# Performance work log

Measured on AMD Instinct MI355X. Metric: run time of the kernel, lower is better.

Reference implementation:

```python
import jax, jax.numpy as jnp
import numpy as np

N = 50000      # nodes
E = 800000     # edges (before self-loops)
F_IN = 128     # num_node_features
H = 4          # heads
C = 64         # hidden_channels
G = 64         # graphs in batch
OUT = 5


def setup_inputs():
    key = jax.random.key(0)
    ks = jax.random.split(key, 16)
    s = 0.1
    def rn(k, shape, sc=s):
        return jax.random.normal(k, shape, dtype=jnp.float32) * sc
    return {
        "x": rn(ks[0], (N, F_IN), 1.0),
        "edge_index": jax.random.randint(ks[1], (2, E), 0, N, dtype=jnp.int32),
        "batch": jnp.sort(jax.random.randint(ks[2], (N,), 0, G, dtype=jnp.int32)),
        "W1": rn(ks[3], (F_IN, H * C)), "a1s": rn(ks[4], (H, C)), "a1d": rn(ks[5], (H, C)), "b1": jnp.zeros((H * C,), jnp.float32),
        "g1": jnp.ones((H * C,), jnp.float32), "be1": jnp.zeros((H * C,), jnp.float32),
        "W2": rn(ks[6], (H * C, H * C)), "a2s": rn(ks[7], (H, C)), "a2d": rn(ks[8], (H, C)), "b2": jnp.zeros((H * C,), jnp.float32),
        "g2": jnp.ones((H * C,), jnp.float32), "be2": jnp.zeros((H * C,), jnp.float32),
        "W3": rn(ks[9], (H * C, C)), "a3s": rn(ks[10], (1, C)), "a3d": rn(ks[11], (1, C)), "b3": jnp.zeros((C,), jnp.float32),
        "g3": jnp.ones((C,), jnp.float32), "be3": jnp.zeros((C,), jnp.float32),
        "Wg": rn(ks[12], (C, 128)), "bg": jnp.zeros((128,), jnp.float32),
        "Wg2": rn(ks[13], (128, 64)), "bg2": jnp.zeros((64,), jnp.float32),
        "Wo": rn(ks[14], (64, OUT)), "bo": jnp.zeros((OUT,), jnp.float32),
    }


def _layer_norm(x, g, b, eps=1e-5):
    mu = jnp.mean(x, axis=-1, keepdims=True)
    var = jnp.mean((x - mu) ** 2, axis=-1, keepdims=True)
    return (x - mu) * jax.lax.rsqrt(var + eps) * g + b


def _gat_conv(x, src, dst, W, a_s, a_d, b, heads, c, concat):
    # PyG GATConv (eval mode, dropout inactive): linear -> per-edge scores ->
    # segment softmax over incoming edges of each dst -> scatter-sum aggregation.
    n = x.shape[0]
    h = (x @ W).reshape(n, heads, c)                 # [N,H,C]
    alpha_src = jnp.sum(h * a_s, axis=-1)            # [N,H]
    alpha_dst = jnp.sum(h * a_d, axis=-1)            # [N,H]
    e = jax.nn.leaky_relu(alpha_src[src] + alpha_dst[dst], 0.2)   # [E',H]
    emax = jax.ops.segment_max(e, dst, num_segments=n)            # [N,H]
    ex = jnp.exp(e - emax[dst])
    denom = jax.ops.segment_sum(ex, dst, num_segments=n)
    alpha = ex / denom[dst]                          # softmax per dst (self-loops guarantee denom>0)
    out = jax.ops.segment_sum(alpha[:, :, None] * h[src], dst, num_segments=n)  # [N,H,C]
    out = out.reshape(n, heads * c) if concat else out.mean(axis=1)
    return out + b


def reference(x, edge_index, batch, W1, a1s, a1d, b1, g1, be1, W2, a2s, a2d, b2, g2, be2, W3, a3s, a3d, b3, g3, be3, Wg, bg, Wg2, bg2, Wo, bo):
    n = x.shape[0]
    loop = jnp.arange(n, dtype=edge_index.dtype)
    src = jnp.concatenate([edge_index[0], loop])     # GATConv adds self-loops
    dst = jnp.concatenate([edge_index[1], loop])
    h = _gat_conv(x, src, dst, W1, a1s, a1d, b1, H, C, True)
    h = jax.nn.elu(_layer_norm(h, g1, be1))
    h = _gat_conv(h, src, dst, W2, a2s, a2d, b2, H, C, True)
    h = jax.nn.elu(_layer_norm(h, g2, be2))
    h = _gat_conv(h, src, dst, W3, a3s, a3d, b3, 1, C, False)
    h = jax.nn.elu(_layer_norm(h, g3, be3))
    # global_mean_pool over graph ids
    sums = jax.ops.segment_sum(h, batch, num_segments=G)
    cnt = jax.ops.segment_sum(jnp.ones((n,), h.dtype), batch, num_segments=G)
    gm = sums / jnp.maximum(cnt, 1.0)[:, None]
    z = jax.nn.relu(gm @ Wg + bg)
    z = jax.nn.relu(z @ Wg2 + bg2)
    return z @ Wo + bo
```

## Files before the change

### kernel.cpp

```cpp
#include <hip/hip_runtime.h>
#include <math.h>

typedef _Float16 half2v __attribute__((ext_vector_type(2)));
typedef _Float16 half4v __attribute__((ext_vector_type(4)));
typedef _Float16 half8v __attribute__((ext_vector_type(8)));
typedef float floatx4 __attribute__((ext_vector_type(4)));

static __device__ __forceinline__ half2v pack_rtz(float a, float b) {
  return __builtin_bit_cast(half2v, __builtin_amdgcn_cvt_pkrtz(a, b));
}

__global__ void cvt16_kernel(const float* __restrict__ in, _Float16* __restrict__ out, int n8) {
  int i = blockIdx.x * 256 + threadIdx.x;
  if (i >= n8) return;
  float4 a = ((const float4*)in)[2 * i];
  float4 b = ((const float4*)in)[2 * i + 1];
  half8v h = {(_Float16)a.x, (_Float16)a.y, (_Float16)a.z, (_Float16)a.w,
              (_Float16)b.x, (_Float16)b.y, (_Float16)b.z, (_Float16)b.w};
  ((half8v*)out)[i] = h;
}

__global__ void wt_kernel(const float* __restrict__ W, _Float16* __restrict__ Wt, int K, int Nc) {
  int col = blockIdx.x;
  int k = threadIdx.x;
  if (k < K) Wt[(size_t)col * K + k] = (_Float16)W[(size_t)k * Nc + col];
}

__global__ void count_kernel(const int* __restrict__ ei, int E, int N, int* __restrict__ counts) {
  int e = blockIdx.x * 256 + threadIdx.x;
  if (e >= E + N) return;
  int d = (e < E) ? ei[E + e] : (e - E);
  atomicAdd(&counts[d], 1);
}

__global__ __launch_bounds__(1024) void scan1_kernel(const int* __restrict__ counts,
                                                     int* __restrict__ offsets,
                                                     int* __restrict__ blocksums, int n) {
  __shared__ int wsum[16];
  int tid = threadIdx.x, lane = tid & 63, wid = tid >> 6;
  int i = blockIdx.x * 1024 + tid;
  int v = (i < n) ? counts[i] : 0;
  int x = v;
  #pragma unroll
  for (int off = 1; off < 64; off <<= 1) {
    int t = __shfl_up(x, off);
    if (lane >= off) x += t;
  }
  if (lane == 63) wsum[wid] = x;
  __syncthreads();
  if (wid == 0) {
    int w = (lane < 16) ? wsum[lane] : 0;
    #pragma unroll
    for (int off = 1; off < 16; off <<= 1) {
      int t = __shfl_up(w, off);
      if (lane >= off) w += t;
    }
    if (lane < 16) wsum[lane] = w;
  }
  __syncthreads();
  int wpre = (wid > 0) ? wsum[wid - 1] : 0;
  if (i < n) offsets[i] = wpre + x - v;
  if (tid == 0) blocksums[blockIdx.x] = wsum[15];
}

__global__ __launch_bounds__(1024) void scan2_kernel(int* __restrict__ blocksums,
                                                     int* __restrict__ offsets, int nb, int n) {
  __shared__ int wsum[16];
  int tid = threadIdx.x, lane = tid & 63, wid = tid >> 6;
  int v = (tid < nb) ? blocksums[tid] : 0;
  int x = v;
  #pragma unroll
  for (int off = 1; off < 64; off <<= 1) {
    int t = __shfl_up(x, off);
    if (lane >= off) x += t;
  }
  if (lane == 63) wsum[wid] = x;
  __syncthreads();
  if (wid == 0) {
    int w = (lane < 16) ? wsum[lane] : 0;
    #pragma unroll
    for (int off = 1; off < 16; off <<= 1) {
      int t = __shfl_up(w, off);
      if (lane >= off) w += t;
    }
    if (lane < 16) wsum[lane] = w;
  }
  __syncthreads();
  int wpre = (wid > 0) ? wsum[wid - 1] : 0;
  if (tid < nb) blocksums[tid] = wpre + x - v;
  if (tid == 0) offsets[n] = wsum[15];
}

__global__ void scan3_kernel(int* __restrict__ offsets, int* __restrict__ cursor,
                             const int* __restrict__ blocksums, int n) {
  int i = blockIdx.x * 256 + threadIdx.x;
  if (i < n) {
    int o = offsets[i] + blocksums[i >> 10];
    offsets[i] = o;
    cursor[i] = o;
  }
}

__global__ void scatter_kernel(const int* __restrict__ ei, int E, int N,
                               int* __restrict__ cursor, int* __restrict__ src_csr) {
  int e = blockIdx.x * 256 + threadIdx.x;
  if (e >= E + N) return;
  int s = (e < E) ? ei[e] : (e - E);
  int d = (e < E) ? ei[E + e] : (e - E);
  int pos = atomicAdd(&cursor[d], 1);
  src_csr[pos] = s;
}

template <int NT, int H>
__global__ __launch_bounds__(256) void gemm16_kernel(const _Float16* __restrict__ A,
                                                     const _Float16* __restrict__ Wt,
                                                     const float* __restrict__ als,
                                                     const float* __restrict__ ald,
                                                     _Float16* __restrict__ out16,
                                                     float* __restrict__ asrc,
                                                     float* __restrict__ adst,
                                                     int M, int K) {
  constexpr int Nc = NT * 16;
  constexpr int BM = 128, BK = 32;
  constexpr int CPH = NT / H;
  __shared__ _Float16 As[BM][40];
  __shared__ _Float16 Ws[Nc][40];
  int bm = blockIdx.x * BM;
  int tid = threadIdx.x;
  int w = tid >> 6, l = tid & 63;
  int lr = l & 15, lg = l >> 4;

  floatx4 acc[2][NT];
  #pragma unroll
  for (int rf = 0; rf < 2; ++rf)
    #pragma unroll
    for (int ct = 0; ct < NT; ++ct) acc[rf][ct] = (floatx4){0.f, 0.f, 0.f, 0.f};

  for (int k0 = 0; k0 < K; k0 += BK) {
    #pragma unroll
    for (int i = 0; i < 2; ++i) {
      int idx = tid + i * 256;
      int r = idx >> 2, c8 = idx & 3;
      int gr = bm + r;
      half8v hv = {(_Float16)0, (_Float16)0, (_Float16)0, (_Float16)0,
                   (_Float16)0, (_Float16)0, (_Float16)0, (_Float16)0};
      if (gr < M) hv = *(const half8v*)&A[(size_t)gr * K + k0 + c8 * 8];
      *(half8v*)&As[r][c8 * 8] = hv;
    }
    #pragma unroll
    for (int i = 0; i < NT / 4; ++i) {
      int idx = tid + i * 256;
      int col = idx >> 2, c8 = idx & 3;
      *(half8v*)&Ws[col][c8 * 8] = *(const half8v*)&Wt[(size_t)col * K + k0 + c8 * 8];
    }
    __syncthreads();
    half8v a0 = *(half8v*)&As[w * 32 + lr][lg * 8];
    half8v a1 = *(half8v*)&As[w * 32 + 16 + lr][lg * 8];
    #pragma unroll
    for (int ct = 0; ct < NT; ++ct) {
      half8v b = *(half8v*)&Ws[ct * 16 + lr][lg * 8];
      acc[0][ct] = __builtin_amdgcn_mfma_f32_16x16x32_f16(a0, b, acc[0][ct], 0, 0, 0);
      acc[1][ct] = __builtin_amdgcn_mfma_f32_16x16x32_f16(a1, b, acc[1][ct], 0, 0, 0);
    }
    __syncthreads();
  }
  float als_r[NT], ald_r[NT];
  #pragma unroll
  for (int ct = 0; ct < NT; ++ct) {
    als_r[ct] = als[ct * 16 + lr];
    ald_r[ct] = ald[ct * 16 + lr];
  }
  #pragma unroll
  for (int rf = 0; rf < 2; ++rf)
    #pragma unroll
    for (int q = 0; q < 4; ++q) {
      int row = bm + w * 32 + rf * 16 + lg * 4 + q;
      float ps[H], pd[H];
      #pragma unroll
      for (int hh = 0; hh < H; ++hh) {
        float s = 0.f, d = 0.f;
        #pragma unroll
        for (int c2 = 0; c2 < CPH; ++c2) {
          int ct = hh * CPH + c2;
          s += acc[rf][ct][q] * als_r[ct];
          d += acc[rf][ct][q] * ald_r[ct];
        }
        ps[hh] = s; pd[hh] = d;
      }
      #pragma unroll
      for (int off = 1; off < 16; off <<= 1) {
        #pragma unroll
        for (int hh = 0; hh < H; ++hh) {
          ps[hh] += __shfl_xor(ps[hh], off);
          pd[hh] += __shfl_xor(pd[hh], off);
        }
      }
      if (row < M) {
        if (lr == 0) {
          #pragma unroll
          for (int hh = 0; hh < H; ++hh) asrc[row * H + hh] = ps[hh];
        } else if (lr == 1) {
          #pragma unroll
          for (int hh = 0; hh < H; ++hh) adst[row * H + hh] = pd[hh];
        }
        #pragma unroll
        for (int ct = 0; ct < NT; ++ct)
          out16[(size_t)row * Nc + ct * 16 + lr] = (_Float16)acc[rf][ct][q];
      }
    }
}

__global__ __launch_bounds__(256) void agg4_ln_kernel(const _Float16* __restrict__ h16,
                                                      const float* __restrict__ asrc,
                                                      const float* __restrict__ adst,
                                                      const int* __restrict__ offsets,
                                                      const int* __restrict__ src_csr,
                                                      const float* __restrict__ bias,
                                                      const float* __restrict__ g,
                                                      const float* __restrict__ be,
                                                      _Float16* __restrict__ out, int n) {
  int wid = threadIdx.x >> 6, lane = threadIdx.x & 63;
  int node = blockIdx.x * 4 + wid;
  if (node >= n) return;
  int start = offsets[node], end = offsets[node + 1];
  int hl = lane >> 5;
  int l5 = lane & 31;
  int head = l5 >> 3;
  float adh = adst[node * 4 + head];
  const uint4* h4 = (const uint4*)h16;
  const half2v ones = {(_Float16)1.f, (_Float16)1.f};
  float acc[8] = {0.f, 0.f, 0.f, 0.f, 0.f, 0.f, 0.f, 0.f};
  float denom = 0.f;
  int i = start + hl;
  for (; i + 2 < end; i += 4) {
    int s0 = src_csr[i], s1 = src_csr[i + 2];
    float sc0 = asrc[s0 * 4 + head] + adh;
    float sc1 = asrc[s1 * 4 + head] + adh;
    sc0 = (sc0 >= 0.f) ? sc0 : 0.2f * sc0;
    sc1 = (sc1 >= 0.f) ? sc1 : 0.2f * sc1;
    float w0 = __expf(sc0), w1 = __expf(sc1);
    uint4 x = h4[(size_t)s0 * 32 + l5];
    uint4 y = h4[(size_t)s1 * 32 + l5];
    half2v w01 = pack_rtz(w0, w1);
    denom = __builtin_amdgcn_fdot2(w01, ones, denom, false);
    acc[0] = __builtin_amdgcn_fdot2(w01, __builtin_bit_cast(half2v, __builtin_amdgcn_perm(y.x, x.x, 0x05040100u)), acc[0], false);
    acc[1] = __builtin_amdgcn_fdot2(w01, __builtin_bit_cast(half2v, __builtin_amdgcn_perm(y.x, x.x, 0x07060302u)), acc[1], false);
    acc[2] = __builtin_amdgcn_fdot2(w01, __builtin_bit_cast(half2v, __builtin_amdgcn_perm(y.y, x.y, 0x05040100u)), acc[2], false);
    acc[3] = __builtin_amdgcn_fdot2(w01, __builtin_bit_cast(half2v, __builtin_amdgcn_perm(y.y, x.y, 0x07060302u)), acc[3], false);
    acc[4] = __builtin_amdgcn_fdot2(w01, __builtin_bit_cast(half2v, __builtin_amdgcn_perm(y.z, x.z, 0x05040100u)), acc[4], false);
    acc[5] = __builtin_amdgcn_fdot2(w01, __builtin_bit_cast(half2v, __builtin_amdgcn_perm(y.z, x.z, 0x07060302u)), acc[5], false);
    acc[6] = __builtin_amdgcn_fdot2(w01, __builtin_bit_cast(half2v, __builtin_amdgcn_perm(y.w, x.w, 0x05040100u)), acc[6], false);
    acc[7] = __builtin_amdgcn_fdot2(w01, __builtin_bit_cast(half2v, __builtin_amdgcn_perm(y.w, x.w, 0x07060302u)), acc[7], false);
  }
  if (i < end) {
    int s0 = src_csr[i];
    float sc0 = asrc[s0 * 4 + head] + adh;
    sc0 = (sc0 >= 0.f) ? sc0 : 0.2f * sc0;
    float w0 = __expf(sc0);
    uint4 x = h4[(size_t)s0 * 32 + l5];
    half2v w01 = pack_rtz(w0, 0.f);
    denom = __builtin_amdgcn_fdot2(w01, ones, denom, false);
    acc[0] = __builtin_amdgcn_fdot2(w01, __builtin_bit_cast(half2v, __builtin_amdgcn_perm(x.x, x.x, 0x05040100u)), acc[0], false);
    acc[1] = __builtin_amdgcn_fdot2(w01, __builtin_bit_cast(half2v, __builtin_amdgcn_perm(x.x, x.x, 0x07060302u)), acc[1], false);
    acc[2] = __builtin_amdgcn_fdot2(w01, __builtin_bit_cast(half2v, __builtin_amdgcn_perm(x.y, x.y, 0x05040100u)), acc[2], false);
    acc[3] = __builtin_amdgcn_fdot2(w01, __builtin_bit_cast(half2v, __builtin_amdgcn_perm(x.y, x.y, 0x07060302u)), acc[3], false);
    acc[4] = __builtin_amdgcn_fdot2(w01, __builtin_bit_cast(half2v, __builtin_amdgcn_perm(x.z, x.z, 0x05040100u)), acc[4], false);
    acc[5] = __builtin_amdgcn_fdot2(w01, __builtin_bit_cast(half2v, __builtin_amdgcn_perm(x.z, x.z, 0x07060302u)), acc[5], false);
    acc[6] = __builtin_amdgcn_fdot2(w01, __builtin_bit_cast(half2v, __builtin_amdgcn_perm(x.w, x.w, 0x05040100u)), acc[6], false);
    acc[7] = __builtin_amdgcn_fdot2(w01, __builtin_bit_cast(half2v, __builtin_amdgcn_perm(x.w, x.w, 0x07060302u)), acc[7], false);
  }
  #pragma unroll
  for (int j = 0; j < 8; ++j) acc[j] += __shfl_xor(acc[j], 32);
  denom += __shfl_xor(denom, 32);
  float inv = 1.f / denom;
  float o[8];
  float4 b0 = *(const float4*)&bias[l5 * 8];
  float4 b1 = *(const float4*)&bias[l5 * 8 + 4];
  o[0] = acc[0] * inv + b0.x; o[1] = acc[1] * inv + b0.y;
  o[2] = acc[2] * inv + b0.z; o[3] = acc[3] * inv + b0.w;
  o[4] = acc[4] * inv + b1.x; o[5] = acc[5] * inv + b1.y;
  o[6] = acc[6] * inv + b1.z; o[7] = acc[7] * inv + b1.w;
  float s = 0.f;
  #pragma unroll
  for (int j = 0; j < 8; ++j) s += o[j];
  #pragma unroll
  for (int off = 16; off; off >>= 1) s += __shfl_xor(s, off);
  float mu = s * (1.f / 256.f);
  float var = 0.f;
  #pragma unroll
  for (int j = 0; j < 8; ++j) { float d = o[j] - mu; var += d * d; }
  #pragma unroll
  for (int off = 16; off; off >>= 1) var += __shfl_xor(var, off);
  float r = rsqrtf(var * (1.f / 256.f) + 1e-5f);
  float4 g0 = *(const float4*)&g[l5 * 8];
  float4 g1 = *(const float4*)&g[l5 * 8 + 4];
  float4 e0 = *(const float4*)&be[l5 * 8];
  float4 e1 = *(const float4*)&be[l5 * 8 + 4];
  float gg[8] = {g0.x, g0.y, g0.z, g0.w, g1.x, g1.y, g1.z, g1.w};
  float ee[8] = {e0.x, e0.y, e0.z, e0.w, e1.x, e1.y, e1.z, e1.w};
  if (hl == 0) {
    half8v yv;
    #pragma unroll
    for (int j = 0; j < 8; ++j) {
      float t = (o[j] - mu) * r * gg[j] + ee[j];
      t = (t > 0.f) ? t : expm1f(t);
      yv[j] = (_Float16)t;
    }
    *(half8v*)&out[(size_t)node * 256 + l5 * 8] = yv;
  }
}

__global__ __launch_bounds__(256) void agg1_ln_kernel(const _Float16* __restrict__ h16,
                                                      const float* __restrict__ asrc,
                                                      const float* __restrict__ adst,
                                                      const int* __restrict__ offsets,
                                                      const int* __restrict__ src_csr,
                                                      const float* __restrict__ bias,
                                                      const float* __restrict__ g,
                                                      const float* __restrict__ be,
                                                      float* __restrict__ out, int n) {
  int wid = threadIdx.x >> 6, lane = threadIdx.x & 63;
  int node = blockIdx.x * 4 + wid;
  if (node >= n) return;
  int start = offsets[node], end = offsets[node + 1];
  int qi = lane >> 4;
  int ql = lane & 15;
  float adh = adst[node];
  const uint2* h2 = (const uint2*)h16;
  const half2v ones = {(_Float16)1.f, (_Float16)1.f};
  float acc[4] = {0.f, 0.f, 0.f, 0.f};
  float denom = 0.f;
  int i = start + qi;
  for (; i + 4 < end; i += 8) {
    int s0 = src_csr[i], s1 = src_csr[i + 4];
    float sc0 = asrc[s0] + adh;
    float sc1 = asrc[s1] + adh;
    sc0 = (sc0 >= 0.f) ? sc0 : 0.2f * sc0;
    sc1 = (sc1 >= 0.f) ? sc1 : 0.2f * sc1;
    float w0 = __expf(sc0), w1 = __expf(sc1);
    uint2 x = h2[(size_t)s0 * 16 + ql];
    uint2 y = h2[(size_t)s1 * 16 + ql];
    half2v w01 = pack_rtz(w0, w1);
    denom = __builtin_amdgcn_fdot2(w01, ones, denom, false);
    acc[0] = __builtin_amdgcn_fdot2(w01, __builtin_bit_cast(half2v, __builtin_amdgcn_perm(y.x, x.x, 0x05040100u)), acc[0], false);
    acc[1] = __builtin_amdgcn_fdot2(w01, __builtin_bit_cast(half2v, __builtin_amdgcn_perm(y.x, x.x, 0x07060302u)), acc[1], false);
    acc[2] = __builtin_amdgcn_fdot2(w01, __builtin_bit_cast(half2v, __builtin_amdgcn_perm(y.y, x.y, 0x05040100u)), acc[2], false);
    acc[3] = __builtin_amdgcn_fdot2(w01, __builtin_bit_cast(half2v, __builtin_amdgcn_perm(y.y, x.y, 0x07060302u)), acc[3], false);
  }
  if (i < end) {
    int s0 = src_csr[i];
    float sc0 = asrc[s0] + adh;
    sc0 = (sc0 >= 0.f) ? sc0 : 0.2f * sc0;
    float w0 = __expf(sc0);
    uint2 x = h2[(size_t)s0 * 16 + ql];
    half2v w01 = pack_rtz(w0, 0.f);
    denom = __builtin_amdgcn_fdot2(w01, ones, denom, false);
    acc[0] = __builtin_amdgcn_fdot2(w01, __builtin_bit_cast(half2v, __builtin_amdgcn_perm(x.x, x.x, 0x05040100u)), acc[0], false);
    acc[1] = __builtin_amdgcn_fdot2(w01, __builtin_bit_cast(half2v, __builtin_amdgcn_perm(x.x, x.x, 0x07060302u)), acc[1], false);
    acc[2] = __builtin_amdgcn_fdot2(w01, __builtin_bit_cast(half2v, __builtin_amdgcn_perm(x.y, x.y, 0x05040100u)), acc[2], false);
    acc[3] = __builtin_amdgcn_fdot2(w01, __builtin_bit_cast(half2v, __builtin_amdgcn_perm(x.y, x.y, 0x07060302u)), acc[3], false);
  }
  #pragma unroll
  for (int off = 32; off >= 16; off >>= 1) {
    #pragma unroll
    for (int j = 0; j < 4; ++j) acc[j] += __shfl_xor(acc[j], off);
    denom += __shfl_xor(denom, off);
  }
  float inv = 1.f / denom;
  float4 b4 = *(const float4*)&bias[ql * 4];
  float o[4];
  o[0] = acc[0] * inv + b4.x; o[1] = acc[1] * inv + b4.y;
  o[2] = acc[2] * inv + b4.z; o[3] = acc[3] * inv + b4.w;
  float s = o[0] + o[1] + o[2] + o[3];
  #pragma unroll
  for (int off = 8; off; off >>= 1) s += __shfl_xor(s, off);
  float mu = s * (1.f / 64.f);
  float var = 0.f;
  #pragma unroll
  for (int j = 0; j < 4; ++j) { float d = o[j] - mu; var += d * d; }
  #pragma unroll
  for (int off = 8; off; off >>= 1) var += __shfl_xor(var, off);
  float r = rsqrtf(var * (1.f / 64.f) + 1e-5f);
  float4 g4 = *(const float4*)&g[ql * 4];
  float4 e4 = *(const float4*)&be[ql * 4];
  float gg[4] = {g4.x, g4.y, g4.z, g4.w};
  float ee[4] = {e4.x, e4.y, e4.z, e4.w};
  float y[4];
  #pragma unroll
  for (int j = 0; j < 4; ++j) {
    float t = (o[j] - mu) * r * gg[j] + ee[j];
    y[j] = (t > 0.f) ? t : expm1f(t);
  }
  if (qi == 0) {
    *(float4*)&out[(size_t)node * 64 + ql * 4] = make_float4(y[0], y[1], y[2], y[3]);
  }
}

__global__ __launch_bounds__(256) void graph_head_kernel(const float* __restrict__ h,
                                                         const int* __restrict__ batch, int N,
                                                         const float* __restrict__ Wg,
                                                         const float* __restrict__ bg,
                                                         const float* __restrict__ Wg2,
                                                         const float* __restrict__ bg2,
                                                         const float* __restrict__ Wo,
                                                         const float* __restrict__ bo,
                                                         float* __restrict__ out) {
  __shared__ int bounds[2];
  __shared__ float part[4][64];
  __shared__ float gm[64];
  __shared__ float z1[128];
  __shared__ float z2[64];
  int g = blockIdx.x;
  int tid = threadIdx.x;
  if (tid < 2) {
    int target = g + tid;
    int lo = 0, hi = N;
    while (lo < hi) {
      int mid = (lo + hi) >> 1;
      if (batch[mid] < target) lo = mid + 1; else hi = mid;
    }
    bounds[tid] = lo;
  }
  __syncthreads();
  int lo = bounds[0], hi = bounds[1];
  int c = tid & 63, sub = tid >> 6;
  float acc = 0.f;
  for (int r = lo + sub; r < hi; r += 4) acc += h[(size_t)r * 64 + c];
  part[sub][c] = acc;
  __syncthreads();
  float invc = 1.f / fmaxf((float)(hi - lo), 1.f);
  if (tid < 64) gm[tid] = (part[0][tid] + part[1][tid] + part[2][tid] + part[3][tid]) * invc;
  __syncthreads();
  if (tid < 128) {
    float a = bg[tid];
    for (int k = 0; k < 64; ++k) a += gm[k] * Wg[k * 128 + tid];
    z1[tid] = fmaxf(a, 0.f);
  }
  __syncthreads();
  if (tid < 64) {
    float a = bg2[tid];
    for (int k = 0; k < 128; ++k) a += z1[k] * Wg2[k * 64 + tid];
    z2[tid] = fmaxf(a, 0.f);
  }
  __syncthreads();
  if (tid < 5) {
    float a = bo[tid];
    for (int k = 0; k < 64; ++k) a += z2[k] * Wo[k * 5 + tid];
    out[g * 5 + tid] = a;
  }
}

extern "C" void kernel_launch(void* const* d_in, const int* in_sizes, int n_in,
                              void* d_out, int out_size, void* d_ws, size_t ws_size,
                              hipStream_t stream) {
  const float* x   = (const float*)d_in[0];
  const int* ei    = (const int*)d_in[1];
  const int* batch = (const int*)d_in[2];
  const float* W1  = (const float*)d_in[3];
  const float* a1s = (const float*)d_in[4];
  const float* a1d = (const float*)d_in[5];
  const float* b1  = (const float*)d_in[6];
  const float* g1  = (const float*)d_in[7];
  const float* be1 = (const float*)d_in[8];
  const float* W2  = (const float*)d_in[9];
  const float* a2s = (const float*)d_in[10];
  const float* a2d = (const float*)d_in[11];
  const float* b2  = (const float*)d_in[12];
  const float* g2  = (const float*)d_in[13];
  const float* be2 = (const float*)d_in[14];
  const float* W3  = (const float*)d_in[15];
  const float* a3s = (const float*)d_in[16];
  const float* a3d = (const float*)d_in[17];
  const float* b3  = (const float*)d_in[18];
  const float* g3  = (const float*)d_in[19];
  const float* be3 = (const float*)d_in[20];
  const float* Wg  = (const float*)d_in[21];
  const float* bg  = (const float*)d_in[22];
  const float* Wg2 = (const float*)d_in[23];
  const float* bg2 = (const float*)d_in[24];
  const float* Wo  = (const float*)d_in[25];
  const float* bo  = (const float*)d_in[26];

  const int N = in_sizes[2];
  const int E = in_sizes[1] / 2;
  const int ET = E + N;
  const int G = 64;
  const int NB = (N + 1023) / 1024;

  char* ws = (char*)d_ws;
  size_t off = 0;
  auto carve = [&](size_t bytes) {
    void* p = ws + off;
    off = (off + bytes + 255) & ~(size_t)255;
    return p;
  };
  int* counts    = (int*)carve((size_t)N * 4);
  int* offsets   = (int*)carve((size_t)(N + 1) * 4);
  int* cursor    = (int*)carve((size_t)N * 4);
  int* blocksums = (int*)carve((size_t)NB * 4);
  int* src_csr   = (int*)carve((size_t)ET * 4);
  float* asrc    = (float*)carve((size_t)N * 4 * 4);
  float* adst    = (float*)carve((size_t)N * 4 * 4);
  _Float16* x16  = (_Float16*)carve((size_t)N * 128 * 2);
  _Float16* a16  = (_Float16*)carve((size_t)N * 256 * 2);
  _Float16* h16  = (_Float16*)carve((size_t)N * 256 * 2);
  float* buf3    = (float*)carve((size_t)N * 64 * 4);
  _Float16* Wt1  = (_Float16*)carve((size_t)128 * 256 * 2);
  _Float16* Wt2  = (_Float16*)carve((size_t)256 * 256 * 2);
  _Float16* Wt3  = (_Float16*)carve((size_t)256 * 64 * 2);
  (void)ws_size;

  const int egrid = (ET + 255) / 256;
  const int ngrid4 = (N + 3) / 4;
  const int mblocks = (N + 127) / 128;

  wt_kernel<<<256, 256, 0, stream>>>(W1, Wt1, 128, 256);
  wt_kernel<<<256, 256, 0, stream>>>(W2, Wt2, 256, 256);
  wt_kernel<<<64, 256, 0, stream>>>(W3, Wt3, 256, 64);
  cvt16_kernel<<<(N * 16 + 255) / 256, 256, 0, stream>>>(x, x16, N * 16);

  hipMemsetAsync(counts, 0, (size_t)N * 4, stream);
  count_kernel<<<egrid, 256, 0, stream>>>(ei, E, N, counts);
  scan1_kernel<<<NB, 1024, 0, stream>>>(counts, offsets, blocksums, N);
  scan2_kernel<<<1, 1024, 0, stream>>>(blocksums, offsets, NB, N);
  scan3_kernel<<<(N + 255) / 256, 256, 0, stream>>>(offsets, cursor, blocksums, N);
  scatter_kernel<<<egrid, 256, 0, stream>>>(ei, E, N, cursor, src_csr);

  gemm16_kernel<16, 4><<<mblocks, 256, 0, stream>>>(x16, Wt1, a1s, a1d, h16, asrc, adst, N, 128);
  agg4_ln_kernel<<<ngrid4, 256, 0, stream>>>(h16, asrc, adst, offsets, src_csr, b1, g1, be1, a16, N);

  gemm16_kernel<16, 4><<<mblocks, 256, 0, stream>>>(a16, Wt2, a2s, a2d, h16, asrc, adst, N, 256);
  agg4_ln_kernel<<<ngrid4, 256, 0, stream>>>(h16, asrc, adst, offsets, src_csr, b2, g2, be2, a16, N);

  gemm16_kernel<4, 1><<<mblocks, 256, 0, stream>>>(a16, Wt3, a3s, a3d, h16, asrc, adst, N, 256);
  agg1_ln_kernel<<<ngrid4, 256, 0, stream>>>(h16, asrc, adst, offsets, src_csr, b3, g3, be3, buf3, N);

  graph_head_kernel<<<G, 256, 0, stream>>>(buf3, batch, N, Wg, bg, Wg2, bg2, Wo, bo,
                                           (float*)d_out);
}
```

Measured before the change: 417.9 us.

## Unroll aggregation loops deeper, shrink agg blocks, merge prep kernels

The edge-gather loops in both aggregation kernels are unrolled to handle four edges per half- or quarter-wave per iteration, with the feature gathers issued before the score and exp math so more loads are in flight. The aggregation kernels now launch 128-thread blocks holding two nodes each instead of four. The three weight-transpose kernels and the x fp16 conversion are merged into one launch to cut launch overhead. The deeper unroll raises register pressure, and the smaller blocks double the block count.

Measured after the change: 399.9 us. -4.3%, faster.

```diff
diff --git a/kernel.cpp b/kernel.cpp
--- a/kernel.cpp
+++ b/kernel.cpp
@@ -9,21 +9,38 @@
 static __device__ __forceinline__ half2v pack_rtz(float a, float b) {
   return __builtin_bit_cast(half2v, __builtin_amdgcn_cvt_pkrtz(a, b));
 }
-
-__global__ void cvt16_kernel(const float* __restrict__ in, _Float16* __restrict__ out, int n8) {
-  int i = blockIdx.x * 256 + threadIdx.x;
-  if (i >= n8) return;
-  float4 a = ((const float4*)in)[2 * i];
-  float4 b = ((const float4*)in)[2 * i + 1];
-  half8v h = {(_Float16)a.x, (_Float16)a.y, (_Float16)a.z, (_Float16)a.w,
-              (_Float16)b.x, (_Float16)b.y, (_Float16)b.z, (_Float16)b.w};
-  ((half8v*)out)[i] = h;
-}
-
-__global__ void wt_kernel(const float* __restrict__ W, _Float16* __restrict__ Wt, int K, int Nc) {
-  int col = blockIdx.x;
-  int k = threadIdx.x;
-  if (k < K) Wt[(size_t)col * K + k] = (_Float16)W[(size_t)k * Nc + col];
+static __device__ __forceinline__ float dot2(half2v w, unsigned hi, unsigned lo, unsigned sel, float acc) {
+  return __builtin_amdgcn_fdot2(w, __builtin_bit_cast(half2v, __builtin_amdgcn_perm(hi, lo, sel)), acc, false);
+}
+
+__global__ __launch_bounds__(256) void prep_kernel(const float* __restrict__ W1,
+                                                   const float* __restrict__ W2,
+                                                   const float* __restrict__ W3,
+                                                   const float* __restrict__ x,
+                                                   _Float16* __restrict__ Wt1,
+                                                   _Float16* __restrict__ Wt2,
+                                                   _Float16* __restrict__ Wt3,
+                                                   _Float16* __restrict__ x16, int n8) {
+  int b = blockIdx.x;
+  int t = threadIdx.x;
+  if (b < 256) {
+    if (t < 128) Wt1[(size_t)b * 128 + t] = (_Float16)W1[(size_t)t * 256 + b];
+  } else if (b < 512) {
+    int col = b - 256;
+    Wt2[(size_t)col * 256 + t] = (_Float16)W2[(size_t)t * 256 + col];
+  } else if (b < 576) {
+    int col = b - 512;
+    Wt3[(size_t)col * 256 + t] = (_Float16)W3[(size_t)t * 64 + col];
+  } else {
+    int i = (b - 576) * 256 + t;
+    if (i < n8) {
+      float4 a = ((const float4*)x)[2 * i];
+      float4 c = ((const float4*)x)[2 * i + 1];
+      half8v h = {(_Float16)a.x, (_Float16)a.y, (_Float16)a.z, (_Float16)a.w,
+                  (_Float16)c.x, (_Float16)c.y, (_Float16)c.z, (_Float16)c.w};
+      ((half8v*)x16)[i] = h;
+    }
+  }
 }
 
 __global__ void count_kernel(const int* __restrict__ ei, int E, int N, int* __restrict__ counts) {
@@ -210,7 +227,7 @@
     }
 }
 
-__global__ __launch_bounds__(256) void agg4_ln_kernel(const _Float16* __restrict__ h16,
+__global__ __launch_bounds__(128) void agg4_ln_kernel(const _Float16* __restrict__ h16,
                                                       const float* __restrict__ asrc,
                                                       const float* __restrict__ adst,
                                                       const int* __restrict__ offsets,
@@ -220,7 +237,7 @@
                                                       const float* __restrict__ be,
                                                       _Float16* __restrict__ out, int n) {
   int wid = threadIdx.x >> 6, lane = threadIdx.x & 63;
-  int node = blockIdx.x * 4 + wid;
+  int node = blockIdx.x * 2 + wid;
   if (node >= n) return;
   int start = offsets[node], end = offsets[node + 1];
   int hl = lane >> 5;
@@ -232,42 +249,75 @@
   float acc[8] = {0.f, 0.f, 0.f, 0.f, 0.f, 0.f, 0.f, 0.f};
   float denom = 0.f;
   int i = start + hl;
+  for (; i + 6 < end; i += 8) {
+    int s0 = src_csr[i], s1 = src_csr[i + 2], s2 = src_csr[i + 4], s3 = src_csr[i + 6];
+    uint4 x0 = h4[(size_t)s0 * 32 + l5];
+    uint4 x1 = h4[(size_t)s1 * 32 + l5];
+    uint4 x2 = h4[(size_t)s2 * 32 + l5];
+    uint4 x3 = h4[(size_t)s3 * 32 + l5];
+    float sc0 = asrc[s0 * 4 + head] + adh;
+    float sc1 = asrc[s1 * 4 + head] + adh;
+    float sc2 = asrc[s2 * 4 + head] + adh;
+    float sc3 = asrc[s3 * 4 + head] + adh;
+    sc0 = (sc0 >= 0.f) ? sc0 : 0.2f * sc0;
+    sc1 = (sc1 >= 0.f) ? sc1 : 0.2f * sc1;
+    sc2 = (sc2 >= 0.f) ? sc2 : 0.2f * sc2;
+    sc3 = (sc3 >= 0.f) ? sc3 : 0.2f * sc3;
+    half2v wa = pack_rtz(__expf(sc0), __expf(sc1));
+    half2v wb = pack_rtz(__expf(sc2), __expf(sc3));
+    denom = __builtin_amdgcn_fdot2(wa, ones, denom, false);
+    denom = __builtin_amdgcn_fdot2(wb, ones, denom, false);
+    acc[0] = dot2(wa, x1.x, x0.x, 0x05040100u, acc[0]);
+    acc[1] = dot2(wa, x1.x, x0.x, 0x07060302u, acc[1]);
+    acc[2] = dot2(wa, x1.y, x0.y, 0x05040100u, acc[2]);
+    acc[3] = dot2(wa, x1.y, x0.y, 0x07060302u, acc[3]);
+    acc[4] = dot2(wa, x1.z, x0.z, 0x05040100u, acc[4]);
+    acc[5] = dot2(wa, x1.z, x0.z, 0x07060302u, acc[5]);
+    acc[6] = dot2(wa, x1.w, x0.w, 0x05040100u, acc[6]);
+    acc[7] = dot2(wa, x1.w, x0.w, 0x07060302u, acc[7]);
+    acc[0] = dot2(wb, x3.x, x2.x, 0x05040100u, acc[0]);
+    acc[1] = dot2(wb, x3.x, x2.x, 0x07060302u, acc[1]);
+    acc[2] = dot2(wb, x3.y, x2.y, 0x05040100u, acc[2]);
+    acc[3] = dot2(wb, x3.y, x2.y, 0x07060302u, acc[3]);
+    acc[4] = dot2(wb, x3.z, x2.z, 0x05040100u, acc[4]);
+    acc[5] = dot2(wb, x3.z, x2.z, 0x07060302u, acc[5]);
+    acc[6] = dot2(wb, x3.w, x2.w, 0x05040100u, acc[6]);
+    acc[7] = dot2(wb, x3.w, x2.w, 0x07060302u, acc[7]);
+  }
   for (; i + 2 < end; i += 4) {
     int s0 = src_csr[i], s1 = src_csr[i + 2];
+    uint4 x0 = h4[(size_t)s0 * 32 + l5];
+    uint4 x1 = h4[(size_t)s1 * 32 + l5];
     float sc0 = asrc[s0 * 4 + head] + adh;
     float sc1 = asrc[s1 * 4 + head] + adh;
     sc0 = (sc0 >= 0.f) ? sc0 : 0.2f * sc0;
     sc1 = (sc1 >= 0.f) ? sc1 : 0.2f * sc1;
-    float w0 = __expf(sc0), w1 = __expf(sc1);
-    uint4 x = h4[(size_t)s0 * 32 + l5];
-    uint4 y = h4[(size_t)s1 * 32 + l5];
-    half2v w01 = pack_rtz(w0, w1);
-    denom = __builtin_amdgcn_fdot2(w01, ones, denom, false);
-    acc[0] = __builtin_amdgcn_fdot2(w01, __builtin_bit_cast(half2v, __builtin_amdgcn_perm(y.x, x.x, 0x05040100u)), acc[0], false);
-    acc[1] = __builtin_amdgcn_fdot2(w01, __builtin_bit_cast(half2v, __builtin_amdgcn_perm(y.x, x.x, 0x07060302u)), acc[1], false);
-    acc[2] = __builtin_amdgcn_fdot2(w01, __builtin_bit_cast(half2v, __builtin_amdgcn_perm(y.y, x.y, 0x05040100u)), acc[2], false);
-    acc[3] = __builtin_amdgcn_fdot2(w01, __builtin_bit_cast(half2v, __builtin_amdgcn_perm(y.y, x.y, 0x07060302u)), acc[3], false);
-    acc[4] = __builtin_amdgcn_fdot2(w01, __builtin_bit_cast(half2v, __builtin_amdgcn_perm(y.z, x.z, 0x05040100u)), acc[4], false);
-    acc[5] = __builtin_amdgcn_fdot2(w01, __builtin_bit_cast(half2v, __builtin_amdgcn_perm(y.z, x.z, 0x07060302u)), acc[5], false);
-    acc[6] = __builtin_amdgcn_fdot2(w01, __builtin_bit_cast(half2v, __builtin_amdgcn_perm(y.w, x.w, 0x05040100u)), acc[6], false);
-    acc[7] = __builtin_amdgcn_fdot2(w01, __builtin_bit_cast(half2v, __builtin_amdgcn_perm(y.w, x.w, 0x07060302u)), acc[7], false);
+    half2v wa = pack_rtz(__expf(sc0), __expf(sc1));
+    denom = __builtin_amdgcn_fdot2(wa, ones, denom, false);
+    acc[0] = dot2(wa, x1.x, x0.x, 0x05040100u, acc[0]);
+    acc[1] = dot2(wa, x1.x, x0.x, 0x07060302u, acc[1]);
+    acc[2] = dot2(wa, x1.y, x0.y, 0x05040100u, acc[2]);
+    acc[3] = dot2(wa, x1.y, x0.y, 0x07060302u, acc[3]);
+    acc[4] = dot2(wa, x1.z, x0.z, 0x05040100u, acc[4]);
+    acc[5] = dot2(wa, x1.z, x0.z, 0x07060302u, acc[5]);
+    acc[6] = dot2(wa, x1.w, x0.w, 0x05040100u, acc[6]);
+    acc[7] = dot2(wa, x1.w, x0.w, 0x07060302u, acc[7]);
   }
   if (i < end) {
     int s0 = src_csr[i];
+    uint4 x0 = h4[(size_t)s0 * 32 + l5];
     float sc0 = asrc[s0 * 4 + head] + adh;
     sc0 = (sc0 >= 0.f) ? sc0 : 0.2f * sc0;
-    float w0 = __expf(sc0);
-    uint4 x = h4[(size_t)s0 * 32 + l5];
-    half2v w01 = pack_rtz(w0, 0.f);
-    denom = __builtin_amdgcn_fdot2(w01, ones, denom, false);
-    acc[0] = __builtin_amdgcn_fdot2(w01, __builtin_bit_cast(half2v, __builtin_amdgcn_perm(x.x, x.x, 0x05040100u)), acc[0], false);
-    acc[1] = __builtin_amdgcn_fdot2(w01, __builtin_bit_cast(half2v, __builtin_amdgcn_perm(x.x, x.x, 0x07060302u)), acc[1], false);
-    acc[2] = __builtin_amdgcn_fdot2(w01, __builtin_bit_cast(half2v, __builtin_amdgcn_perm(x.y, x.y, 0x05040100u)), acc[2], false);
-    acc[3] = __builtin_amdgcn_fdot2(w01, __builtin_bit_cast(half2v, __builtin_amdgcn_perm(x.y, x.y, 0x07060302u)), acc[3], false);
-    acc[4] = __builtin_amdgcn_fdot2(w01, __builtin_bit_cast(half2v, __builtin_amdgcn_perm(x.z, x.z, 0x05040100u)), acc[4], false);
-    acc[5] = __builtin_amdgcn_fdot2(w01, __builtin_bit_cast(half2v, __builtin_amdgcn_perm(x.z, x.z, 0x07060302u)), acc[5], false);
-    acc[6] = __builtin_amdgcn_fdot2(w01, __builtin_bit_cast(half2v, __builtin_amdgcn_perm(x.w, x.w, 0x05040100u)), acc[6], false);
-    acc[7] = __builtin_amdgcn_fdot2(w01, __builtin_bit_cast(half2v, __builtin_amdgcn_perm(x.w, x.w, 0x07060302u)), acc[7], false);
+    half2v wa = pack_rtz(__expf(sc0), 0.f);
+    denom = __builtin_amdgcn_fdot2(wa, ones, denom, false);
+    acc[0] = dot2(wa, x0.x, x0.x, 0x05040100u, acc[0]);
+    acc[1] = dot2(wa, x0.x, x0.x, 0x07060302u, acc[1]);
+    acc[2] = dot2(wa, x0.y, x0.y, 0x05040100u, acc[2]);
+    acc[3] = dot2(wa, x0.y, x0.y, 0x07060302u, acc[3]);
+    acc[4] = dot2(wa, x0.z, x0.z, 0x05040100u, acc[4]);
+    acc[5] = dot2(wa, x0.z, x0.z, 0x07060302u, acc[5]);
+    acc[6] = dot2(wa, x0.w, x0.w, 0x05040100u, acc[6]);
+    acc[7] = dot2(wa, x0.w, x0.w, 0x07060302u, acc[7]);
   }
   #pragma unroll
   for (int j = 0; j < 8; ++j) acc[j] += __shfl_xor(acc[j], 32);
@@ -310,7 +360,7 @@
   }
 }
 
-__global__ __launch_bounds__(256) void agg1_ln_kernel(const _Float16* __restrict__ h16,
+__global__ __launch_bounds__(128) void agg1_ln_kernel(const _Float16* __restrict__ h16,
                                                       const float* __restrict__ asrc,
                                                       const float* __restrict__ adst,
                                                       const int* __restrict__ offsets,
@@ -320,7 +370,7 @@
                                                       const float* __restrict__ be,
                                                       float* __restrict__ out, int n) {
   int wid = threadIdx.x >> 6, lane = threadIdx.x & 63;
-  int node = blockIdx.x * 4 + wid;
+  int node = blockIdx.x * 2 + wid;
   if (node >= n) return;
   int start = offsets[node], end = offsets[node + 1];
   int qi = lane >> 4;
@@ -331,34 +381,59 @@
   float acc[4] = {0.f, 0.f, 0.f, 0.f};
   float denom = 0.f;
   int i = start + qi;
+  for (; i + 12 < end; i += 16) {
+    int s0 = src_csr[i], s1 = src_csr[i + 4], s2 = src_csr[i + 8], s3 = src_csr[i + 12];
+    uint2 x0 = h2[(size_t)s0 * 16 + ql];
+    uint2 x1 = h2[(size_t)s1 * 16 + ql];
+    uint2 x2 = h2[(size_t)s2 * 16 + ql];
+    uint2 x3 = h2[(size_t)s3 * 16 + ql];
+    float sc0 = asrc[s0] + adh;
+    float sc1 = asrc[s1] + adh;
+    float sc2 = asrc[s2] + adh;
+    float sc3 = asrc[s3] + adh;
+    sc0 = (sc0 >= 0.f) ? sc0 : 0.2f * sc0;
+    sc1 = (sc1 >= 0.f) ? sc1 : 0.2f * sc1;
+    sc2 = (sc2 >= 0.f) ? sc2 : 0.2f * sc2;
+    sc3 = (sc3 >= 0.f) ? sc3 : 0.2f * sc3;
+    half2v wa = pack_rtz(__expf(sc0), __expf(sc1));
+    half2v wb = pack_rtz(__expf(sc2), __expf(sc3));
+    denom = __builtin_amdgcn_fdot2(wa, ones, denom, false);
+    denom = __builtin_amdgcn_fdot2(wb, ones, denom, false);
+    acc[0] = dot2(wa, x1.x, x0.x, 0x05040100u, acc[0]);
+    acc[1] = dot2(wa, x1.x, x0.x, 0x07060302u, acc[1]);
+    acc[2] = dot2(wa, x1.y, x0.y, 0x05040100u, acc[2]);
+    acc[3] = dot2(wa, x1.y, x0.y, 0x07060302u, acc[3]);
+    acc[0] = dot2(wb, x3.x, x2.x, 0x05040100u, acc[0]);
+    acc[1] = dot2(wb, x3.x, x2.x, 0x07060302u, acc[1]);
+    acc[2] = dot2(wb, x3.y, x2.y, 0x05040100u, acc[2]);
+    acc[3] = dot2(wb, x3.y, x2.y, 0x07060302u, acc[3]);
+  }
   for (; i + 4 < end; i += 8) {
     int s0 = src_csr[i], s1 = src_csr[i + 4];
+    uint2 x0 = h2[(size_t)s0 * 16 + ql];
+    uint2 x1 = h2[(size_t)s1 * 16 + ql];
     float sc0 = asrc[s0] + adh;
     float sc1 = asrc[s1] + adh;
     sc0 = (sc0 >= 0.f) ? sc0 : 0.2f * sc0;
     sc1 = (sc1 >= 0.f) ? sc1 : 0.2f * sc1;
-    float w0 = __expf(sc0), w1 = __expf(sc1);
-    uint2 x = h2[(size_t)s0 * 16 + ql];
-    uint2 y = h2[(size_t)s1 * 16 + ql];
-    half2v w01 = pack_rtz(w0, w1);
-    denom = __builtin_amdgcn_fdot2(w01, ones, denom, false);
-    acc[0] = __builtin_amdgcn_fdot2(w01, __builtin_bit_cast(half2v, __builtin_amdgcn_perm(y.x, x.x, 0x05040100u)), acc[0], false);
-    acc[1] = __builtin_amdgcn_fdot2(w01, __builtin_bit_cast(half2v, __builtin_amdgcn_perm(y.x, x.x, 0x07060302u)), acc[1], false);
-    acc[2] = __builtin_amdgcn_fdot2(w01, __builtin_bit_cast(half2v, __builtin_amdgcn_perm(y.y, x.y, 0x05040100u)), acc[2], false);
-    acc[3] = __builtin_amdgcn_fdot2(w01, __builtin_bit_cast(half2v, __builtin_amdgcn_perm(y.y, x.y, 0x07060302u)), acc[3], false);
+    half2v wa = pack_rtz(__expf(sc0), __expf(sc1));
+    denom = __builtin_amdgcn_fdot2(wa, ones, denom, false);
+    acc[0] = dot2(wa, x1.x, x0.x, 0x05040100u, acc[0]);
+    acc[1] = dot2(wa, x1.x, x0.x, 0x07060302u, acc[1]);
+    acc[2] = dot2(wa, x1.y, x0.y, 0x05040100u, acc[2]);
+    acc[3] = dot2(wa, x1.y, x0.y, 0x07060302u, acc[3]);
   }
   if (i < end) {
     int s0 = src_csr[i];
+    uint2 x0 = h2[(size_t)s0 * 16 + ql];
     float sc0 = asrc[s0] + adh;
     sc0 = (sc0 >= 0.f) ? sc0 : 0.2f * sc0;
-    float w0 = __expf(sc0);
-    uint2 x = h2[(size_t)s0 * 16 + ql];
-    half2v w01 = pack_rtz(w0, 0.f);
-    denom = __builtin_amdgcn_fdot2(w01, ones, denom, false);
-    acc[0] = __builtin_amdgcn_fdot2(w01, __builtin_bit_cast(half2v, __builtin_amdgcn_perm(x.x, x.x, 0x05040100u)), acc[0], false);
-    acc[1] = __builtin_amdgcn_fdot2(w01, __builtin_bit_cast(half2v, __builtin_amdgcn_perm(x.x, x.x, 0x07060302u)), acc[1], false);
-    acc[2] = __builtin_amdgcn_fdot2(w01, __builtin_bit_cast(half2v, __builtin_amdgcn_perm(x.y, x.y, 0x05040100u)), acc[2], false);
-    acc[3] = __builtin_amdgcn_fdot2(w01, __builtin_bit_cast(half2v, __builtin_amdgcn_perm(x.y, x.y, 0x07060302u)), acc[3], false);
+    half2v wa = pack_rtz(__expf(sc0), 0.f);
+    denom = __builtin_amdgcn_fdot2(wa, ones, denom, false);
+    acc[0] = dot2(wa, x0.x, x0.x, 0x05040100u, acc[0]);
+    acc[1] = dot2(wa, x0.x, x0.x, 0x07060302u, acc[1]);
+    acc[2] = dot2(wa, x0.y, x0.y, 0x05040100u, acc[2]);
+    acc[3] = dot2(wa, x0.y, x0.y, 0x07060302u, acc[3]);
   }
   #pragma unroll
   for (int off = 32; off >= 16; off >>= 1) {
@@ -511,13 +586,11 @@
   (void)ws_size;
 
   const int egrid = (ET + 255) / 256;
-  const int ngrid4 = (N + 3) / 4;
+  const int ngrid2 = (N + 1) / 2;
   const int mblocks = (N + 127) / 128;
-
-  wt_kernel<<<256, 256, 0, stream>>>(W1, Wt1, 128, 256);
-  wt_kernel<<<256, 256, 0, stream>>>(W2, Wt2, 256, 256);
-  wt_kernel<<<64, 256, 0, stream>>>(W3, Wt3, 256, 64);
-  cvt16_kernel<<<(N * 16 + 255) / 256, 256, 0, stream>>>(x, x16, N * 16);
+  const int ncvt = (N * 16 + 255) / 256;
+
+  prep_kernel<<<576 + ncvt, 256, 0, stream>>>(W1, W2, W3, x, Wt1, Wt2, Wt3, x16, N * 16);
 
   hipMemsetAsync(counts, 0, (size_t)N * 4, stream);
   count_kernel<<<egrid, 256, 0, stream>>>(ei, E, N, counts);
@@ -527,13 +600,13 @@
   scatter_kernel<<<egrid, 256, 0, stream>>>(ei, E, N, cursor, src_csr);
 
   gemm16_kernel<16, 4><<<mblocks, 256, 0, stream>>>(x16, Wt1, a1s, a1d, h16, asrc, adst, N, 128);
-  agg4_ln_kernel<<<ngrid4, 256, 0, stream>>>(h16, asrc, adst, offsets, src_csr, b1, g1, be1, a16, N);
+  agg4_ln_kernel<<<ngrid2, 128, 0, stream>>>(h16, asrc, adst, offsets, src_csr, b1, g1, be1, a16, N);
 
   gemm16_kernel<16, 4><<<mblocks, 256, 0, stream>>>(a16, Wt2, a2s, a2d, h16, asrc, adst, N, 256);
-  agg4_ln_kernel<<<ngrid4, 256, 0, stream>>>(h16, asrc, adst, offsets, src_csr, b2, g2, be2, a16, N);
+  agg4_ln_kernel<<<ngrid2, 128, 0, stream>>>(h16, asrc, adst, offsets, src_csr, b2, g2, be2, a16, N);
 
   gemm16_kernel<4, 1><<<mblocks, 256, 0, stream>>>(a16, Wt3, a3s, a3d, h16, asrc, adst, N, 256);
-  agg1_ln_kernel<<<ngrid4, 256, 0, stream>>>(h16, asrc, adst, offsets, src_csr, b3, g3, be3, buf3, N);
+  agg1_ln_kernel<<<ngrid2, 128, 0, stream>>>(h16, asrc, adst, offsets, src_csr, b3, g3, be3, buf3, N);
 
   graph_head_kernel<<<G, 256, 0, stream>>>(buf3, batch, N, Wg, bg, Wg2, bg2, Wo, bo,
                                            (float*)d_out);
```
